# Kernel optimization log

Measured on AMD Instinct MI355X. Metric: run time of the kernel, lower is better.

Reference implementation:

```python
import jax, jax.numpy as jnp
import numpy as np

HIGH_PERCENT = 0.1          # fraction of elements kept at high bit-width
LOW_BIT, HIGH_BIT = 1, 8
MAXQ_LOW = 2 ** LOW_BIT - 1
MAXQ_HIGH = 2 ** HIGH_BIT - 1
ROWS, COLS = 4096, 11008    # LLaMA-7B MLP weight


def setup_inputs() -> dict:
    key = jax.random.key(0)
    k1, k2, k3 = jax.random.split(key, 3)
    x = jax.random.normal(k1, (ROWS, COLS), jnp.float32) * 0.02
    # per-channel (per-row) scales; symmetric -> zero = (maxq+1)/2
    scale_low = jax.random.uniform(k2, (ROWS, 1), jnp.float32, 0.005, 0.02)
    scale_high = jax.random.uniform(k3, (ROWS, 1), jnp.float32, 0.0005, 0.002)
    zero_low = jnp.full((ROWS, 1), (MAXQ_LOW + 1) / 2.0, jnp.float32)
    zero_high = jnp.full((ROWS, 1), (MAXQ_HIGH + 1) / 2.0, jnp.float32)
    return {"x": x, "scale_low": scale_low, "zero_low": zero_low,
            "scale_high": scale_high, "zero_high": zero_high}


def _affine_qdq(x, scale, zero, maxq):
    # GPTQ-style quantize: scale * (clamp(round(x/scale) + zero, 0, maxq) - zero)
    q = jnp.clip(jnp.round(x / scale) + zero, 0.0, float(maxq))
    return scale * (q - zero)


def reference(x, scale_low, zero_low, scale_high, zero_high):
    n = x.size
    high_num = int(n * HIGH_PERCENT)
    k_lo = high_num // 2  # torch.kthvalue is 1-indexed -> sorted[k-1]
    xs = jnp.sort(x.reshape(-1))
    low_thresh = xs[k_lo - 1]
    high_thresh = xs[n - high_num // 2 - 1]
    mask = (x > low_thresh) & (x < high_thresh)  # True = low-magnitude bulk
    x1 = _affine_qdq(x * mask, scale_low, zero_low, MAXQ_LOW)
    x2 = _affine_qdq(x * (~mask), scale_high, zero_high, MAXQ_HIGH)
    return x1 + x2
```

## Files before the change

kernel.cpp:

```cpp
#include <hip/hip_runtime.h>
#include <stdint.h>

#define ROWS 4096
#define COLS 11008
#define NTOT (ROWS * COLS)
#define NV4  (NTOT / 4)
#define COLS4 (COLS / 4)

#define HIGH_NUM 4508876u
#define RANK_LO  (HIGH_NUM / 2u)
#define RANK_HI  ((unsigned)NTOT - HIGH_NUM / 2u)

#define BLK 256
#define GRID 2048
#define NTHR (GRID * BLK)
#define NTILES 11008

#define SAMPLES 4194304ull
#define RS_LO ((unsigned)(((unsigned long long)RANK_LO * SAMPLES) / (unsigned long long)NTOT))
#define RS_HI ((unsigned)(((unsigned long long)RANK_HI * SAMPLES) / (unsigned long long)NTOT))

#define WSZ_KEYS (2u << 20)

#define OFF_CLO   0
#define OFF_CHI   64
#define OFF_META  128
#define OFF_THR   132
#define OFF_H1S   256
#define OFF_CSUM  (OFF_H1S + 4096)
#define OFF_WLO   (OFF_CSUM + 4096)
#define OFF_WHI   (OFF_WLO + WSZ_KEYS)
#define WS_WORDS  (OFF_WHI + WSZ_KEYS)

typedef float vfloat4 __attribute__((ext_vector_type(4)));

__device__ __forceinline__ unsigned f2key(float f) {
    unsigned u = __float_as_uint(f);
    return (u & 0x80000000u) ? ~u : (u | 0x80000000u);
}
__device__ __forceinline__ float key2f(unsigned key) {
    unsigned u = (key & 0x80000000u) ? (key & 0x7fffffffu) : ~key;
    return __uint_as_float(u);
}

__device__ __forceinline__ float qdq(float xx, bool m, float sl, float zl, float sh, float zh) {
    float s  = m ? sl : sh;
    float z  = m ? zl : zh;
    float mq = m ? 1.0f : 255.0f;
    float q = rintf(xx / s) + z;
    q = fminf(fmaxf(q, 0.0f), mq);
    return s * (q - z);
}

__global__ void __launch_bounds__(BLK) sample_kernel(const float* __restrict__ x,
                                                     unsigned* __restrict__ ws) {
    __shared__ unsigned h[8192];
    for (int i = threadIdx.x; i < 8192; i += BLK) h[i] = 0u;
    __syncthreads();

    const float4* x4 = (const float4*)x;
    const unsigned base = blockIdx.x * 11008u;
    const int par = threadIdx.x & 1;
#pragma unroll
    for (int i = 0; i < 4; i++) {
        float4 v = x4[base + threadIdx.x + 256 * i];
        atomicAdd(&h[((f2key(v.x) >> 20) << 1) + par], 1u);
        atomicAdd(&h[((f2key(v.y) >> 20) << 1) + par], 1u);
        atomicAdd(&h[((f2key(v.z) >> 20) << 1) + par], 1u);
        atomicAdd(&h[((f2key(v.w) >> 20) << 1) + par], 1u);
    }
    __syncthreads();
    unsigned* hist = ws + OFF_H1S;
    for (int i = threadIdx.x; i < 4096; i += BLK) {
        unsigned c = h[2 * i] + h[2 * i + 1];
        if (c) atomicAdd(&hist[i], c);
    }
}

__global__ void __launch_bounds__(BLK) scan_sample_kernel(unsigned* __restrict__ ws) {
    __shared__ unsigned part[256];
    const unsigned* hist = ws + OFF_H1S;
    unsigned* meta = ws + OFF_META;
    int t = threadIdx.x;
    unsigned v[16];
    unsigned sum = 0u;
#pragma unroll
    for (int i = 0; i < 16; i++) { v[i] = hist[t * 16 + i]; sum += v[i]; }
    part[t] = sum;
    __syncthreads();
    for (int off = 1; off < 256; off <<= 1) {
        unsigned a = (t >= off) ? part[t - off] : 0u;
        __syncthreads();
        part[t] += a;
        __syncthreads();
    }
    unsigned incl = part[t];
    unsigned excl = incl - sum;
    unsigned ranks[2] = {RS_LO, RS_HI};
    for (int k = 0; k < 2; k++) {
        unsigned Rs = ranks[k];
        if (excl < Rs && incl >= Rs) {
            unsigned cum = excl;
            for (int i = 0; i < 16; i++) {
                if (cum + v[i] >= Rs) {
                    unsigned b = (unsigned)(t * 16 + i);
                    unsigned rel = Rs - cum;
                    unsigned wb = (2u * rel <= v[i]) ? (b > 0 ? b - 1 : 0) : b;
                    if (wb > 4094u) wb = 4094u;
                    meta[k] = wb << 20;
                    break;
                }
                cum += v[i];
            }
        }
    }
}

__device__ __forceinline__ void passA_elem(float f, unsigned wlo, unsigned whi,
                                           unsigned& cLo, unsigned& cHi,
                                           unsigned* hLo, unsigned* hHi) {
    unsigned key = f2key(f);
    cLo += (key < wlo) ? 1u : 0u;
    cHi += (key < whi) ? 1u : 0u;
    unsigned dlo = key - wlo;
    if (dlo < WSZ_KEYS) atomicAdd(&hLo[dlo], 1u);
    unsigned dhi = key - whi;
    if (dhi < WSZ_KEYS) atomicAdd(&hHi[dhi], 1u);
}

__global__ void __launch_bounds__(BLK) passA_kernel(const float* __restrict__ x,
                                                    unsigned* __restrict__ ws) {
    const unsigned wlo = __builtin_amdgcn_readfirstlane(ws[OFF_META + 0]);
    const unsigned whi = __builtin_amdgcn_readfirstlane(ws[OFF_META + 1]);
    unsigned* hLo = ws + OFF_WLO;
    unsigned* hHi = ws + OFF_WHI;

    const float4* x4 = (const float4*)x;
    unsigned cLo = 0u, cHi = 0u;

    for (unsigned tile = blockIdx.x; tile < NTILES; tile += gridDim.x) {
        const float4* p = x4 + (size_t)tile * 1024u + threadIdx.x;
        float4 a = p[0];
        float4 b = p[256];
        float4 c = p[512];
        float4 d = p[768];
        passA_elem(a.x, wlo, whi, cLo, cHi, hLo, hHi);
        passA_elem(a.y, wlo, whi, cLo, cHi, hLo, hHi);
        passA_elem(a.z, wlo, whi, cLo, cHi, hLo, hHi);
        passA_elem(a.w, wlo, whi, cLo, cHi, hLo, hHi);
        passA_elem(b.x, wlo, whi, cLo, cHi, hLo, hHi);
        passA_elem(b.y, wlo, whi, cLo, cHi, hLo, hHi);
        passA_elem(b.z, wlo, whi, cLo, cHi, hLo, hHi);
        passA_elem(b.w, wlo, whi, cLo, cHi, hLo, hHi);
        passA_elem(c.x, wlo, whi, cLo, cHi, hLo, hHi);
        passA_elem(c.y, wlo, whi, cLo, cHi, hLo, hHi);
        passA_elem(c.z, wlo, whi, cLo, cHi, hLo, hHi);
        passA_elem(c.w, wlo, whi, cLo, cHi, hLo, hHi);
        passA_elem(d.x, wlo, whi, cLo, cHi, hLo, hHi);
        passA_elem(d.y, wlo, whi, cLo, cHi, hLo, hHi);
        passA_elem(d.z, wlo, whi, cLo, cHi, hLo, hHi);
        passA_elem(d.w, wlo, whi, cLo, cHi, hLo, hHi);
    }

    __shared__ unsigned red[256];
    red[threadIdx.x] = cLo;
    for (int off = 128; off > 0; off >>= 1) {
        __syncthreads();
        if (threadIdx.x < off) red[threadIdx.x] += red[threadIdx.x + off];
    }
    if (threadIdx.x == 0) atomicAdd(&ws[OFF_CLO + (blockIdx.x & 63)], red[0]);
    __syncthreads();
    red[threadIdx.x] = cHi;
    for (int off = 128; off > 0; off >>= 1) {
        __syncthreads();
        if (threadIdx.x < off) red[threadIdx.x] += red[threadIdx.x + off];
    }
    if (threadIdx.x == 0) atomicAdd(&ws[OFF_CHI + (blockIdx.x & 63)], red[0]);
}

__global__ void __launch_bounds__(BLK) chunksum_kernel(unsigned* __restrict__ ws) {
    const unsigned* p = ws + OFF_WLO + (size_t)blockIdx.x * 1024;
    int t = threadIdx.x;
    unsigned s = p[t] + p[t + 256] + p[t + 512] + p[t + 768];
    __shared__ unsigned red[256];
    red[t] = s;
    for (int off = 128; off > 0; off >>= 1) {
        __syncthreads();
        if (t < off) red[t] += red[t + off];
    }
    if (t == 0) ws[OFF_CSUM + blockIdx.x] = red[0];
}

__global__ void __launch_bounds__(BLK) scanB_kernel(unsigned* __restrict__ ws) {
    __shared__ unsigned part[256];
    __shared__ unsigned s_C, s_c, s_r;
    const int t = threadIdx.x;
    const int tgt = blockIdx.x;
    float* thr = (float*)(ws + OFF_THR);

    part[t] = (t < 64) ? ws[(tgt ? OFF_CHI : OFF_CLO) + t] : 0u;
    for (int off = 128; off > 0; off >>= 1) {
        __syncthreads();
        if (t < off) part[t] += part[t + off];
    }
    if (t == 0) s_C = part[0];
    __syncthreads();
    const unsigned RANK = tgt ? RANK_HI : RANK_LO;
    const unsigned R = RANK - s_C;
    __syncthreads();

    const unsigned* cs = ws + OFF_CSUM + tgt * 2048;
    unsigned v[8];
    unsigned sum = 0u;
#pragma unroll
    for (int i = 0; i < 8; i++) { v[i] = cs[t * 8 + i]; sum += v[i]; }
    part[t] = sum;
    __syncthreads();
    for (int off = 1; off < 256; off <<= 1) {
        unsigned a = (t >= off) ? part[t - off] : 0u;
        __syncthreads();
        part[t] += a;
        __syncthreads();
    }
    {
        unsigned incl = part[t], excl = incl - sum;
        if (excl < R && incl >= R) {
            unsigned cum = excl;
            for (int i = 0; i < 8; i++) {
                if (cum + v[i] >= R) { s_c = (unsigned)(t * 8 + i); s_r = R - cum; break; }
                cum += v[i];
            }
        }
    }
    __syncthreads();
    const unsigned c  = s_c;
    const unsigned R2 = s_r;
    __syncthreads();

    const unsigned* hp = ws + OFF_WLO + (size_t)tgt * WSZ_KEYS + (size_t)c * 1024;
    unsigned w[4];
    unsigned sum2 = 0u;
#pragma unroll
    for (int i = 0; i < 4; i++) { w[i] = hp[t * 4 + i]; sum2 += w[i]; }
    part[t] = sum2;
    __syncthreads();
    for (int off = 1; off < 256; off <<= 1) {
        unsigned a = (t >= off) ? part[t - off] : 0u;
        __syncthreads();
        part[t] += a;
        __syncthreads();
    }
    {
        unsigned incl = part[t], excl = incl - sum2;
        if (excl < R2 && incl >= R2) {
            unsigned cum = excl;
            for (int i = 0; i < 4; i++) {
                if (cum + w[i] >= R2) {
                    unsigned key = ws[OFF_META + tgt] + (c * 1024u + (unsigned)(t * 4 + i));
                    thr[tgt] = key2f(key);
                    break;
                }
                cum += w[i];
            }
        }
    }
}

__global__ void __launch_bounds__(BLK) quant_kernel(const float* __restrict__ x,
                                                    const float* __restrict__ sl_,
                                                    const float* __restrict__ zl_,
                                                    const float* __restrict__ sh_,
                                                    const float* __restrict__ zh_,
                                                    const unsigned* __restrict__ ws,
                                                    float* __restrict__ out) {
    const float lowT  = __uint_as_float(__builtin_amdgcn_readfirstlane(ws[OFF_THR + 0]));
    const float highT = __uint_as_float(__builtin_amdgcn_readfirstlane(ws[OFF_THR + 1]));
    const float4* x4 = (const float4*)x;
    vfloat4* o4 = (vfloat4*)out;

    for (unsigned tile = blockIdx.x; tile < NTILES; tile += gridDim.x) {
        const size_t base = (size_t)tile * 1024u + threadIdx.x;
        float4 vv[4];
        vv[0] = x4[base];
        vv[1] = x4[base + 256];
        vv[2] = x4[base + 512];
        vv[3] = x4[base + 768];
#pragma unroll
        for (int u = 0; u < 4; u++) {
            unsigned j = (unsigned)(base + 256u * u);
            unsigned row = j / COLS4;
            float sl = sl_[row], zl = zl_[row];
            float sh = sh_[row], zh = zh_[row];
            float in[4] = {vv[u].x, vv[u].y, vv[u].z, vv[u].w};
            float r[4];
#pragma unroll
            for (int c = 0; c < 4; c++) {
                float xx = in[c];
                bool m = (xx > lowT) && (xx < highT);
                r[c] = qdq(xx, m, sl, zl, sh, zh);
            }
            vfloat4 rv = {r[0], r[1], r[2], r[3]};
            __builtin_nontemporal_store(rv, &o4[j]);
        }
    }
}

extern "C" void kernel_launch(void* const* d_in, const int* in_sizes, int n_in,
                              void* d_out, int out_size, void* d_ws, size_t ws_size,
                              hipStream_t stream) {
    const float* x  = (const float*)d_in[0];
    const float* sl = (const float*)d_in[1];
    const float* zl = (const float*)d_in[2];
    const float* sh = (const float*)d_in[3];
    const float* zh = (const float*)d_in[4];
    float* out = (float*)d_out;
    unsigned* ws = (unsigned*)d_ws;

    (void)hipMemsetAsync(d_ws, 0, (size_t)WS_WORDS * 4, stream);

    sample_kernel<<<1024, BLK, 0, stream>>>(x, ws);
    scan_sample_kernel<<<1, BLK, 0, stream>>>(ws);
    passA_kernel<<<GRID, BLK, 0, stream>>>(x, ws);
    chunksum_kernel<<<4096, BLK, 0, stream>>>(ws);
    scanB_kernel<<<2, BLK, 0, stream>>>(ws);
    quant_kernel<<<GRID, BLK, 0, stream>>>(x, sl, zl, sh, zh, ws, out);
}
```

Measured before the change: 443.8 us.

## Add fine sampling pass to narrow exact-histogram windows before full pass

Adds a second sampling pass that histograms the sample at 4-key granularity within the coarse window, then scans it to bound the target rank within a confidence margin. The full-data pass then histograms only a much narrower key window (capped at 512K bins instead of 2M). This shrinks the workspace memset, the histogram atomics footprint and the chunk-sum/scan work. In exchange it adds three small kernel launches and an extra read of the sampled data. Correctness now depends on the margin holding, because the width is clamped to WMAX.

```diff
diff --git a/kernel.cpp b/kernel.cpp
--- a/kernel.cpp
+++ b/kernel.cpp
@@ -13,24 +13,29 @@
 
 #define BLK 256
 #define GRID 2048
-#define NTHR (GRID * BLK)
 #define NTILES 11008
 
 #define SAMPLES 4194304ull
 #define RS_LO ((unsigned)(((unsigned long long)RANK_LO * SAMPLES) / (unsigned long long)NTOT))
 #define RS_HI ((unsigned)(((unsigned long long)RANK_HI * SAMPLES) / (unsigned long long)NTOT))
-
-#define WSZ_KEYS (2u << 20)
+#define M_S 4500u
+
+#define FSPAN (2u << 20)
+#define FBINS (1u << 19)
+#define WMAX  (1u << 19)
 
 #define OFF_CLO   0
 #define OFF_CHI   64
 #define OFF_META  128
-#define OFF_THR   132
+#define OFF_THR   144
 #define OFF_H1S   256
-#define OFF_CSUM  (OFF_H1S + 4096)
-#define OFF_WLO   (OFF_CSUM + 4096)
-#define OFF_WHI   (OFF_WLO + WSZ_KEYS)
-#define WS_WORDS  (OFF_WHI + WSZ_KEYS)
+#define OFF_FCS   (OFF_H1S + 4096)
+#define OFF_WCS   (OFF_FCS + 1024)
+#define OFF_FLO   8192
+#define OFF_FHI   (OFF_FLO + FBINS)
+#define OFF_WLO   (OFF_FHI + FBINS)
+#define OFF_WHI   (OFF_WLO + WMAX)
+#define WS_WORDS  (OFF_WHI + WMAX)
 
 typedef float vfloat4 __attribute__((ext_vector_type(4)));
 
@@ -42,7 +47,6 @@
     unsigned u = (key & 0x80000000u) ? (key & 0x7fffffffu) : ~key;
     return __uint_as_float(u);
 }
-
 __device__ __forceinline__ float qdq(float xx, bool m, float sl, float zl, float sh, float zh) {
     float s  = m ? sl : sh;
     float z  = m ? zl : zh;
@@ -57,7 +61,6 @@
     __shared__ unsigned h[8192];
     for (int i = threadIdx.x; i < 8192; i += BLK) h[i] = 0u;
     __syncthreads();
-
     const float4* x4 = (const float4*)x;
     const unsigned base = blockIdx.x * 11008u;
     const int par = threadIdx.x & 1;
@@ -108,6 +111,9 @@
                     unsigned wb = (2u * rel <= v[i]) ? (b > 0 ? b - 1 : 0) : b;
                     if (wb > 4094u) wb = 4094u;
                     meta[k] = wb << 20;
+                    unsigned Cs = cum;
+                    if (wb < b) Cs -= hist[b - 1];
+                    meta[6 + k] = Cs;
                     break;
                 }
                 cum += v[i];
@@ -116,22 +122,135 @@
     }
 }
 
-__device__ __forceinline__ void passA_elem(float f, unsigned wlo, unsigned whi,
+__global__ void __launch_bounds__(BLK) sample_fine_kernel(const float* __restrict__ x,
+                                                          unsigned* __restrict__ ws) {
+    const unsigned w0 = __builtin_amdgcn_readfirstlane(ws[OFF_META + 0]);
+    const unsigned w1 = __builtin_amdgcn_readfirstlane(ws[OFF_META + 1]);
+    unsigned* f0 = ws + OFF_FLO;
+    unsigned* f1 = ws + OFF_FHI;
+    const float4* x4 = (const float4*)x;
+    const unsigned base = blockIdx.x * 11008u;
+#pragma unroll
+    for (int i = 0; i < 4; i++) {
+        float4 v = x4[base + threadIdx.x + 256 * i];
+        float f[4] = {v.x, v.y, v.z, v.w};
+#pragma unroll
+        for (int c = 0; c < 4; c++) {
+            unsigned key = f2key(f[c]);
+            unsigned d0 = key - w0;
+            if (d0 < FSPAN) atomicAdd(&f0[d0 >> 2], 1u);
+            unsigned d1 = key - w1;
+            if (d1 < FSPAN) atomicAdd(&f1[d1 >> 2], 1u);
+        }
+    }
+}
+
+__global__ void __launch_bounds__(BLK) csum_kernel(const unsigned* __restrict__ src,
+                                                   unsigned* __restrict__ dst) {
+    const unsigned* p = src + (size_t)blockIdx.x * 1024;
+    int t = threadIdx.x;
+    unsigned s = p[t] + p[t + 256] + p[t + 512] + p[t + 768];
+    __shared__ unsigned red[256];
+    red[t] = s;
+    for (int off = 128; off > 0; off >>= 1) {
+        __syncthreads();
+        if (t < off) red[t] += red[t + off];
+    }
+    if (t == 0) dst[blockIdx.x] = red[0];
+}
+
+__global__ void __launch_bounds__(BLK) fine_scan_kernel(unsigned* __restrict__ ws) {
+    __shared__ unsigned part[256];
+    __shared__ unsigned sT, sC, sR;
+    __shared__ unsigned sBin[2];
+    const int t = threadIdx.x;
+    const int tgt = blockIdx.x;
+    const unsigned* cs = ws + OFF_FCS + tgt * 512;
+    unsigned c0 = cs[2 * t], c1 = cs[2 * t + 1];
+    unsigned gsum = c0 + c1;
+    part[t] = gsum;
+    __syncthreads();
+    for (int off = 1; off < 256; off <<= 1) {
+        unsigned a = (t >= off) ? part[t - off] : 0u;
+        __syncthreads();
+        part[t] += a;
+        __syncthreads();
+    }
+    if (t == 255) sT = part[255];
+    __syncthreads();
+    const unsigned T = sT;
+    const unsigned incl = part[t], excl = incl - gsum;
+    unsigned Rs = tgt ? RS_HI : RS_LO;
+    unsigned Cs = ws[OFF_META + 6 + tgt];
+    unsigned RsA = Rs - Cs;
+    if (RsA < 1u) RsA = 1u;
+    if (RsA > T) RsA = T;
+    unsigned rA = (RsA > M_S) ? RsA - M_S : 1u;
+    unsigned rB = RsA + M_S;
+    if (rB > T) rB = T;
+
+    for (int q = 0; q < 2; q++) {
+        unsigned r = q ? rB : rA;
+        if (excl < r && incl >= r) {
+            if (excl + c0 >= r) { sC = 2u * t;      sR = r - excl; }
+            else                { sC = 2u * t + 1u; sR = r - excl - c0; }
+        }
+        __syncthreads();
+        unsigned chunk = sC, rr = sR;
+        __syncthreads();
+        const unsigned* hp = ws + OFF_FLO + (size_t)tgt * FBINS + (size_t)chunk * 1024;
+        unsigned w[4];
+        unsigned s2 = 0u;
+#pragma unroll
+        for (int i = 0; i < 4; i++) { w[i] = hp[t * 4 + i]; s2 += w[i]; }
+        part[t] = s2;
+        __syncthreads();
+        for (int off = 1; off < 256; off <<= 1) {
+            unsigned a = (t >= off) ? part[t - off] : 0u;
+            __syncthreads();
+            part[t] += a;
+            __syncthreads();
+        }
+        unsigned incl2 = part[t], excl2 = incl2 - s2;
+        if (excl2 < rr && incl2 >= rr) {
+            unsigned cum = excl2;
+            for (int i = 0; i < 4; i++) {
+                if (cum + w[i] >= rr) { sBin[q] = chunk * 1024u + (unsigned)(t * 4 + i); break; }
+                cum += w[i];
+            }
+        }
+        __syncthreads();
+    }
+    if (t == 0) {
+        unsigned wstart = ws[OFF_META + tgt];
+        unsigned kA = wstart + sBin[0] * 4u;
+        unsigned kB = wstart + (sBin[1] + 1u) * 4u;
+        unsigned width = kB - kA;
+        if (width > WMAX) width = WMAX;
+        ws[OFF_META + 2 + 2 * tgt] = kA;
+        ws[OFF_META + 3 + 2 * tgt] = width;
+    }
+}
+
+__device__ __forceinline__ void passA_elem(float f, unsigned kAlo, unsigned wLo,
+                                           unsigned kAhi, unsigned wHi,
                                            unsigned& cLo, unsigned& cHi,
                                            unsigned* hLo, unsigned* hHi) {
     unsigned key = f2key(f);
-    cLo += (key < wlo) ? 1u : 0u;
-    cHi += (key < whi) ? 1u : 0u;
-    unsigned dlo = key - wlo;
-    if (dlo < WSZ_KEYS) atomicAdd(&hLo[dlo], 1u);
-    unsigned dhi = key - whi;
-    if (dhi < WSZ_KEYS) atomicAdd(&hHi[dhi], 1u);
+    cLo += (key < kAlo) ? 1u : 0u;
+    cHi += (key < kAhi) ? 1u : 0u;
+    unsigned d0 = key - kAlo;
+    if (d0 < wLo) atomicAdd(&hLo[d0], 1u);
+    unsigned d1 = key - kAhi;
+    if (d1 < wHi) atomicAdd(&hHi[d1], 1u);
 }
 
 __global__ void __launch_bounds__(BLK) passA_kernel(const float* __restrict__ x,
                                                     unsigned* __restrict__ ws) {
-    const unsigned wlo = __builtin_amdgcn_readfirstlane(ws[OFF_META + 0]);
-    const unsigned whi = __builtin_amdgcn_readfirstlane(ws[OFF_META + 1]);
+    const unsigned kAlo = __builtin_amdgcn_readfirstlane(ws[OFF_META + 2]);
+    const unsigned wLo  = __builtin_amdgcn_readfirstlane(ws[OFF_META + 3]);
+    const unsigned kAhi = __builtin_amdgcn_readfirstlane(ws[OFF_META + 4]);
+    const unsigned wHi  = __builtin_amdgcn_readfirstlane(ws[OFF_META + 5]);
     unsigned* hLo = ws + OFF_WLO;
     unsigned* hHi = ws + OFF_WHI;
 
@@ -144,22 +263,22 @@
         float4 b = p[256];
         float4 c = p[512];
         float4 d = p[768];
-        passA_elem(a.x, wlo, whi, cLo, cHi, hLo, hHi);
-        passA_elem(a.y, wlo, whi, cLo, cHi, hLo, hHi);
-        passA_elem(a.z, wlo, whi, cLo, cHi, hLo, hHi);
-        passA_elem(a.w, wlo, whi, cLo, cHi, hLo, hHi);
-        passA_elem(b.x, wlo, whi, cLo, cHi, hLo, hHi);
-        passA_elem(b.y, wlo, whi, cLo, cHi, hLo, hHi);
-        passA_elem(b.z, wlo, whi, cLo, cHi, hLo, hHi);
-        passA_elem(b.w, wlo, whi, cLo, cHi, hLo, hHi);
-        passA_elem(c.x, wlo, whi, cLo, cHi, hLo, hHi);
-        passA_elem(c.y, wlo, whi, cLo, cHi, hLo, hHi);
-        passA_elem(c.z, wlo, whi, cLo, cHi, hLo, hHi);
-        passA_elem(c.w, wlo, whi, cLo, cHi, hLo, hHi);
-        passA_elem(d.x, wlo, whi, cLo, cHi, hLo, hHi);
-        passA_elem(d.y, wlo, whi, cLo, cHi, hLo, hHi);
-        passA_elem(d.z, wlo, whi, cLo, cHi, hLo, hHi);
-        passA_elem(d.w, wlo, whi, cLo, cHi, hLo, hHi);
+        passA_elem(a.x, kAlo, wLo, kAhi, wHi, cLo, cHi, hLo, hHi);
+        passA_elem(a.y, kAlo, wLo, kAhi, wHi, cLo, cHi, hLo, hHi);
+        passA_elem(a.z, kAlo, wLo, kAhi, wHi, cLo, cHi, hLo, hHi);
+        passA_elem(a.w, kAlo, wLo, kAhi, wHi, cLo, cHi, hLo, hHi);
+        passA_elem(b.x, kAlo, wLo, kAhi, wHi, cLo, cHi, hLo, hHi);
+        passA_elem(b.y, kAlo, wLo, kAhi, wHi, cLo, cHi, hLo, hHi);
+        passA_elem(b.z, kAlo, wLo, kAhi, wHi, cLo, cHi, hLo, hHi);
+        passA_elem(b.w, kAlo, wLo, kAhi, wHi, cLo, cHi, hLo, hHi);
+        passA_elem(c.x, kAlo, wLo, kAhi, wHi, cLo, cHi, hLo, hHi);
+        passA_elem(c.y, kAlo, wLo, kAhi, wHi, cLo, cHi, hLo, hHi);
+        passA_elem(c.z, kAlo, wLo, kAhi, wHi, cLo, cHi, hLo, hHi);
+        passA_elem(c.w, kAlo, wLo, kAhi, wHi, cLo, cHi, hLo, hHi);
+        passA_elem(d.x, kAlo, wLo, kAhi, wHi, cLo, cHi, hLo, hHi);
+        passA_elem(d.y, kAlo, wLo, kAhi, wHi, cLo, cHi, hLo, hHi);
+        passA_elem(d.z, kAlo, wLo, kAhi, wHi, cLo, cHi, hLo, hHi);
+        passA_elem(d.w, kAlo, wLo, kAhi, wHi, cLo, cHi, hLo, hHi);
     }
 
     __shared__ unsigned red[256];
@@ -178,22 +297,9 @@
     if (threadIdx.x == 0) atomicAdd(&ws[OFF_CHI + (blockIdx.x & 63)], red[0]);
 }
 
-__global__ void __launch_bounds__(BLK) chunksum_kernel(unsigned* __restrict__ ws) {
-    const unsigned* p = ws + OFF_WLO + (size_t)blockIdx.x * 1024;
-    int t = threadIdx.x;
-    unsigned s = p[t] + p[t + 256] + p[t + 512] + p[t + 768];
-    __shared__ unsigned red[256];
-    red[t] = s;
-    for (int off = 128; off > 0; off >>= 1) {
-        __syncthreads();
-        if (t < off) red[t] += red[t + off];
-    }
-    if (t == 0) ws[OFF_CSUM + blockIdx.x] = red[0];
-}
-
 __global__ void __launch_bounds__(BLK) scanB_kernel(unsigned* __restrict__ ws) {
     __shared__ unsigned part[256];
-    __shared__ unsigned s_C, s_c, s_r;
+    __shared__ unsigned s_C, s_chunk, s_r;
     const int t = threadIdx.x;
     const int tgt = blockIdx.x;
     float* thr = (float*)(ws + OFF_THR);
@@ -209,12 +315,10 @@
     const unsigned R = RANK - s_C;
     __syncthreads();
 
-    const unsigned* cs = ws + OFF_CSUM + tgt * 2048;
-    unsigned v[8];
-    unsigned sum = 0u;
-#pragma unroll
-    for (int i = 0; i < 8; i++) { v[i] = cs[t * 8 + i]; sum += v[i]; }
-    part[t] = sum;
+    const unsigned* cs = ws + OFF_WCS + tgt * 512;
+    unsigned c0 = cs[2 * t], c1 = cs[2 * t + 1];
+    unsigned gsum = c0 + c1;
+    part[t] = gsum;
     __syncthreads();
     for (int off = 1; off < 256; off <<= 1) {
         unsigned a = (t >= off) ? part[t - off] : 0u;
@@ -222,27 +326,21 @@
         part[t] += a;
         __syncthreads();
     }
-    {
-        unsigned incl = part[t], excl = incl - sum;
-        if (excl < R && incl >= R) {
-            unsigned cum = excl;
-            for (int i = 0; i < 8; i++) {
-                if (cum + v[i] >= R) { s_c = (unsigned)(t * 8 + i); s_r = R - cum; break; }
-                cum += v[i];
-            }
-        }
-    }
-    __syncthreads();
-    const unsigned c  = s_c;
-    const unsigned R2 = s_r;
-    __syncthreads();
-
-    const unsigned* hp = ws + OFF_WLO + (size_t)tgt * WSZ_KEYS + (size_t)c * 1024;
+    unsigned incl = part[t], excl = incl - gsum;
+    if (excl < R && incl >= R) {
+        if (excl + c0 >= R) { s_chunk = 2u * t;      s_r = R - excl; }
+        else                { s_chunk = 2u * t + 1u; s_r = R - excl - c0; }
+    }
+    __syncthreads();
+    unsigned chunk = s_chunk, rr = s_r;
+    __syncthreads();
+
+    const unsigned* hp = ws + (tgt ? OFF_WHI : OFF_WLO) + (size_t)chunk * 1024;
     unsigned w[4];
-    unsigned sum2 = 0u;
-#pragma unroll
-    for (int i = 0; i < 4; i++) { w[i] = hp[t * 4 + i]; sum2 += w[i]; }
-    part[t] = sum2;
+    unsigned s2 = 0u;
+#pragma unroll
+    for (int i = 0; i < 4; i++) { w[i] = hp[t * 4 + i]; s2 += w[i]; }
+    part[t] = s2;
     __syncthreads();
     for (int off = 1; off < 256; off <<= 1) {
         unsigned a = (t >= off) ? part[t - off] : 0u;
@@ -250,18 +348,16 @@
         part[t] += a;
         __syncthreads();
     }
-    {
-        unsigned incl = part[t], excl = incl - sum2;
-        if (excl < R2 && incl >= R2) {
-            unsigned cum = excl;
-            for (int i = 0; i < 4; i++) {
-                if (cum + w[i] >= R2) {
-                    unsigned key = ws[OFF_META + tgt] + (c * 1024u + (unsigned)(t * 4 + i));
-                    thr[tgt] = key2f(key);
-                    break;
-                }
-                cum += w[i];
+    unsigned incl2 = part[t], excl2 = incl2 - s2;
+    if (excl2 < rr && incl2 >= rr) {
+        unsigned cum = excl2;
+        for (int i = 0; i < 4; i++) {
+            if (cum + w[i] >= rr) {
+                unsigned key = ws[OFF_META + 2 + 2 * tgt] + chunk * 1024u + (unsigned)(t * 4 + i);
+                thr[tgt] = key2f(key);
+                break;
             }
+            cum += w[i];
         }
     }
 }
@@ -320,8 +416,11 @@
 
     sample_kernel<<<1024, BLK, 0, stream>>>(x, ws);
     scan_sample_kernel<<<1, BLK, 0, stream>>>(ws);
+    sample_fine_kernel<<<1024, BLK, 0, stream>>>(x, ws);
+    csum_kernel<<<1024, BLK, 0, stream>>>(ws + OFF_FLO, ws + OFF_FCS);
+    fine_scan_kernel<<<2, BLK, 0, stream>>>(ws);
     passA_kernel<<<GRID, BLK, 0, stream>>>(x, ws);
-    chunksum_kernel<<<4096, BLK, 0, stream>>>(ws);
+    csum_kernel<<<1024, BLK, 0, stream>>>(ws + OFF_WLO, ws + OFF_WCS);
     scanB_kernel<<<2, BLK, 0, stream>>>(ws);
     quant_kernel<<<GRID, BLK, 0, stream>>>(x, sl, zl, sh, zh, ws, out);
 }
```

Result: faster. 391.9 us (-11.7%).
